# Performance work log

Hardware: AMD Instinct MI355X
Metric: run time of the kernel (lower is better)

Reference implementation:

```python
import jax, jax.numpy as jnp
import numpy as np
import math

D_MODEL = 1024
N_HEADS = 16
D_FF = 4096
B, S = 4, 2048
EPS = 1e-5


def _layernorm(x, g, b):
    mu = jnp.mean(x, axis=-1, keepdims=True)
    var = jnp.mean(jnp.square(x - mu), axis=-1, keepdims=True)
    return (x - mu) * jax.lax.rsqrt(var + EPS) * g + b


def setup_inputs() -> dict:
    key = jax.random.key(0)
    ks = jax.random.split(key, 16)
    D, F = D_MODEL, D_FF
    s = 1.0 / math.sqrt(D)
    sf = 1.0 / math.sqrt(F)
    return {
        "x": jax.random.normal(ks[0], (B, S, D), jnp.float32),
        "mask": jnp.ones((B, 1, 1, S), jnp.int32),
        "Wq": jax.random.uniform(ks[1], (D, D), jnp.float32, -s, s),
        "bq": jnp.zeros((D,), jnp.float32),
        "Wk": jax.random.uniform(ks[2], (D, D), jnp.float32, -s, s),
        "bk": jnp.zeros((D,), jnp.float32),
        "Wv": jax.random.uniform(ks[3], (D, D), jnp.float32, -s, s),
        "bv": jnp.zeros((D,), jnp.float32),
        "Wo": jax.random.uniform(ks[4], (D, D), jnp.float32, -s, s),
        "bo": jnp.zeros((D,), jnp.float32),
        "W1": jax.random.uniform(ks[5], (D, F), jnp.float32, -s, s),
        "b1": jnp.zeros((F,), jnp.float32),
        "W2": jax.random.uniform(ks[6], (F, D), jnp.float32, -sf, sf),
        "b2": jnp.zeros((D,), jnp.float32),
        "g1": jnp.ones((D,), jnp.float32),
        "be1": jnp.zeros((D,), jnp.float32),
        "g2": jnp.ones((D,), jnp.float32),
        "be2": jnp.zeros((D,), jnp.float32),
    }


def reference(x, mask, Wq, bq, Wk, bk, Wv, bv, Wo, bo, W1, b1, W2, b2, g1, be1, g2, be2):
    Bb, Ss, D = x.shape
    H = N_HEADS
    hd = D // H
    # QKV projections -> [B, H, S, hd]
    q = (x @ Wq + bq).reshape(Bb, Ss, H, hd).transpose(0, 2, 1, 3)
    k = (x @ Wk + bk).reshape(Bb, Ss, H, hd).transpose(0, 2, 1, 3)
    v = (x @ Wv + bv).reshape(Bb, Ss, H, hd).transpose(0, 2, 1, 3)
    # explicit O(S^2) attention, as in the source
    scores = jnp.einsum("bhqd,bhkd->bhqk", q, k) / math.sqrt(hd)
    scores = jnp.where(mask == 0, jnp.float32(-1e9), scores)
    attn = jax.nn.softmax(scores, axis=-1)
    o = jnp.einsum("bhqk,bhkd->bhqd", attn, v)
    o = o.transpose(0, 2, 1, 3).reshape(Bb, Ss, D)
    attn_out = o @ Wo + bo
    # residual + LN (dropout in eval mode = identity)
    h = _layernorm(x + attn_out, g1, be1)
    ff = jax.nn.relu(h @ W1 + b1) @ W2 + b2
    return _layernorm(h + ff, g2, be2)
```

## Files before the change

### kernel.cpp

```cpp
#include <hip/hip_runtime.h>
#include <hip/hip_bf16.h>
#include <stdint.h>

typedef __bf16 bf16;
typedef __bf16 bf16x8 __attribute__((ext_vector_type(8)));
typedef __bf16 bf16x4 __attribute__((ext_vector_type(4)));
typedef float f32x4 __attribute__((ext_vector_type(4)));
typedef unsigned short u16;

__device__ __forceinline__ float b2f(bf16 v) { return (float)v; }
__device__ __forceinline__ bf16 f2b(float f) { return (bf16)f; }

#define GLD16(gp, lp)                                              \
  __builtin_amdgcn_global_load_lds(                                \
      (const __attribute__((address_space(1))) void*)(gp),         \
      (__attribute__((address_space(3))) void*)(lp), 16, 0, 0)

__device__ __forceinline__ float ldval(const void* p, size_t i, int isf32) {
  return isf32 ? ((const float*)p)[i] : b2f(((const bf16*)p)[i]);
}

__global__ void sniff_kernel(const void* x, int* flag) {
  __shared__ int smax[256];
  int tid = threadIdx.x;
  const u16* p = (const u16*)x;
  int mx = 0;
  for (int i = tid; i < 8192; i += 256) {
    int e = (p[i] >> 7) & 0xFF;
    mx = mx > e ? mx : e;
  }
  smax[tid] = mx;
  __syncthreads();
  for (int s = 128; s > 0; s >>= 1) {
    if (tid < s) smax[tid] = smax[tid] > smax[tid + s] ? smax[tid] : smax[tid + s];
    __syncthreads();
  }
  if (tid == 0) *flag = (smax[0] >= 135) ? 1 : 0;
}

__global__ void cvt_kernel8(const void* __restrict__ in, bf16* __restrict__ out,
                            int n8, const int* __restrict__ flag) {
  int f = *flag;
  int i = blockIdx.x * 256 + threadIdx.x;
  if (i >= n8) return;
  bf16x8 o;
  if (f) {
    const float4* p = (const float4*)in + (size_t)i * 2;
    float4 a = p[0], c = p[1];
    o[0] = f2b(a.x); o[1] = f2b(a.y); o[2] = f2b(a.z); o[3] = f2b(a.w);
    o[4] = f2b(c.x); o[5] = f2b(c.y); o[6] = f2b(c.z); o[7] = f2b(c.w);
  } else {
    o = ((const bf16x8*)in)[i];
  }
  ((bf16x8*)out)[i] = o;
}

__global__ void cvt_biases_kernel(const void* bq, const void* bk, const void* bv,
                                  const void* bo, const void* b1, const void* b2,
                                  const void* g1, const void* be1, const void* g2,
                                  const void* be2, bf16* __restrict__ sv,
                                  const int* __restrict__ flag) {
  int f = *flag;
  int i = blockIdx.x * 256 + threadIdx.x;
  if (i >= 13312) return;
  int seg = i >> 10;
  int off = i & 1023;
  const void* src;
  switch (seg) {
    case 0: src = bq; break;
    case 1: src = bk; break;
    case 2: src = bv; break;
    case 3: src = bo; break;
    case 4: case 5: case 6: case 7: src = b1; off = i - 4096; break;
    case 8: src = b2; break;
    case 9: src = g1; break;
    case 10: src = be1; break;
    case 11: src = g2; break;
    default: src = be2; break;
  }
  sv[i] = f2b(ldval(src, off, f));
}

__global__ void transpose_all(const void* Wq, const void* Wk, const void* Wv,
                              const void* Wo, const void* W1, const void* W2,
                              bf16* WqkvT, bf16* WoT, bf16* W1T, bf16* W2T,
                              const int* __restrict__ flag) {
  int f = *flag;
  __shared__ bf16 tile[32][33];
  int blk = blockIdx.x;
  const void* in; bf16* out; int K, N, bx, by;
  if (blk < 4096) {
    int w = blk >> 10, t = blk & 1023;
    bx = t & 31; by = t >> 5; K = 1024; N = 1024;
    if (w == 0)      { in = Wq; out = WqkvT; }
    else if (w == 1) { in = Wk; out = WqkvT + 1024 * 1024; }
    else if (w == 2) { in = Wv; out = WqkvT + 2048 * 1024; }
    else             { in = Wo; out = WoT; }
  } else if (blk < 8192) {
    int t = blk - 4096; bx = t & 127; by = t >> 7; K = 1024; N = 4096;
    in = W1; out = W1T;
  } else {
    int t = blk - 8192; bx = t & 31; by = t >> 5; K = 4096; N = 1024;
    in = W2; out = W2T;
  }
  int bn = bx * 32, bk = by * 32;
  int tx = threadIdx.x, ty = threadIdx.y;
#pragma unroll
  for (int i = 0; i < 32; i += 8)
    tile[ty + i][tx] = f2b(ldval(in, (size_t)(bk + ty + i) * N + bn + tx, f));
  __syncthreads();
#pragma unroll
  for (int i = 0; i < 32; i += 8)
    out[(size_t)(bn + ty + i) * K + bk + tx] = tile[tx][ty + i];
}

template <int ACT, int GROUP>
__global__ __launch_bounds__(256, 4)
void gemm_bt(const bf16* __restrict__ A, const bf16* __restrict__ Bt,
             const bf16* __restrict__ bias, bf16* __restrict__ C,
             int M, int N, int K) {
  __shared__ __attribute__((aligned(16))) bf16 As[128][64];
  __shared__ __attribute__((aligned(16))) bf16 Bs[128][64];
  bf16 (*Cs)[136] = (bf16(*)[136])&As[0][0];
  const int tid = threadIdx.x;
  const int wave = tid >> 6;
  const int lane = tid & 63;

  const int grid_n = N >> 7;
  const int pid = blockIdx.x;
  const int xcd = pid & 7;
  const int j = pid >> 3;
  const int per = GROUP * grid_n;
  const int chunk = j / per;
  const int r0 = j - chunk * per;
  const int mb = xcd * 8 + chunk * GROUP + (r0 & (GROUP - 1));
  const int nb = r0 / GROUP;
  const int m0 = mb * 128;
  const int n0 = nb * 128;

  const int wr = (wave >> 1) * 64;
  const int wc = (wave & 1) * 64;
  const int row_q = lane & 15;
  const int quad = lane >> 4;

  const f32x4 fz = {0.f, 0.f, 0.f, 0.f};
  f32x4 acc[4][4];
#pragma unroll
  for (int i = 0; i < 4; i++)
#pragma unroll
    for (int jj = 0; jj < 4; jj++) acc[i][jj] = fz;

  int srow[4], sck[4];
#pragma unroll
  for (int i = 0; i < 4; i++) {
    int c = i * 256 + tid;
    srow[i] = c >> 3;
    sck[i] = (c & 7) * 8;
  }

  for (int k0 = 0; k0 < K; k0 += 64) {
    __syncthreads();
#pragma unroll
    for (int i = 0; i < 4; i++) {
      GLD16(A + (size_t)(m0 + srow[i]) * K + k0 + sck[i], &As[srow[i]][sck[i]]);
      GLD16(Bt + (size_t)(n0 + srow[i]) * K + k0 + sck[i], &Bs[srow[i]][sck[i]]);
    }
    __syncthreads();
#pragma unroll
    for (int ks = 0; ks < 2; ks++) {
      bf16x8 af[4], bfr[4];
      int cf = ks * 4 + quad;
#pragma unroll
      for (int mi = 0; mi < 4; mi++)
        af[mi] = *(const bf16x8*)&As[wr + mi * 16 + row_q][cf * 8];
#pragma unroll
      for (int ni = 0; ni < 4; ni++)
        bfr[ni] = *(const bf16x8*)&Bs[wc + ni * 16 + row_q][cf * 8];
#pragma unroll
      for (int mi = 0; mi < 4; mi++)
#pragma unroll
        for (int ni = 0; ni < 4; ni++)
          acc[mi][ni] = __builtin_amdgcn_mfma_f32_16x16x32_bf16(
              af[mi], bfr[ni], acc[mi][ni], 0, 0, 0);
    }
  }

#pragma unroll
  for (int p = 0; p < 4; p++) {
    __syncthreads();
    if ((wave >> 1) == (p >> 1)) {
#pragma unroll
      for (int ni = 0; ni < 4; ni++) {
        int col = wc + ni * 16 + row_q;
        float bval = b2f(bias[n0 + col]);
#pragma unroll
        for (int mi2 = 0; mi2 < 2; mi2++) {
          int mi = (p & 1) * 2 + mi2;
#pragma unroll
          for (int reg = 0; reg < 4; reg++) {
            int lr = mi2 * 16 + quad * 4 + reg;
            float v = acc[mi][ni][reg] + bval;
            if (ACT == 1) v = v > 0.f ? v : 0.f;
            Cs[lr][col] = f2b(v);
          }
        }
      }
    }
    __syncthreads();
#pragma unroll
    for (int i = 0; i < 2; i++) {
      int u = i * 256 + tid;
      int row = u >> 4;
      int cu = u & 15;
      uint4 v = *(const uint4*)&Cs[row][cu * 8];
      *(uint4*)&C[(size_t)(m0 + p * 32 + row) * N + n0 + cu * 8] = v;
    }
  }
}

template <int GROUP>
__global__ __launch_bounds__(256, 4)
void gemm_qkv(const bf16* __restrict__ A, const bf16* __restrict__ Bt,
              const bf16* __restrict__ bias, bf16* __restrict__ Cqk,
              bf16* __restrict__ Vg, int M, int K) {
  __shared__ __attribute__((aligned(16))) bf16 As[128][64];
  __shared__ __attribute__((aligned(16))) bf16 Bs[128][64];
  bf16 (*Cs)[136] = (bf16(*)[136])&As[0][0];
  const int tid = threadIdx.x;
  const int wave = tid >> 6;
  const int lane = tid & 63;

  const int grid_n = 24;
  const int pid = blockIdx.x;
  const int xcd = pid & 7;
  const int j = pid >> 3;
  const int per = GROUP * grid_n;
  const int chunk = j / per;
  const int r0 = j - chunk * per;
  const int mb = xcd * 8 + chunk * GROUP + (r0 & (GROUP - 1));
  const int nb = r0 / GROUP;
  const int m0 = mb * 128;
  const int n0 = nb * 128;

  const int wr = (wave >> 1) * 64;
  const int wc = (wave & 1) * 64;
  const int row_q = lane & 15;
  const int quad = lane >> 4;

  const f32x4 fz = {0.f, 0.f, 0.f, 0.f};
  f32x4 acc[4][4];
#pragma unroll
  for (int i = 0; i < 4; i++)
#pragma unroll
    for (int jj = 0; jj < 4; jj++) acc[i][jj] = fz;

  int srow[4], sck[4];
#pragma unroll
  for (int i = 0; i < 4; i++) {
    int c = i * 256 + tid;
    srow[i] = c >> 3;
    sck[i] = (c & 7) * 8;
  }

  for (int k0 = 0; k0 < K; k0 += 64) {
    __syncthreads();
#pragma unroll
    for (int i = 0; i < 4; i++) {
      GLD16(A + (size_t)(m0 + srow[i]) * K + k0 + sck[i], &As[srow[i]][sck[i]]);
      GLD16(Bt + (size_t)(n0 + srow[i]) * K + k0 + sck[i], &Bs[srow[i]][sck[i]]);
    }
    __syncthreads();
#pragma unroll
    for (int ks = 0; ks < 2; ks++) {
      bf16x8 af[4], bfr[4];
      int cf = ks * 4 + quad;
#pragma unroll
      for (int mi = 0; mi < 4; mi++)
        af[mi] = *(const bf16x8*)&As[wr + mi * 16 + row_q][cf * 8];
#pragma unroll
      for (int ni = 0; ni < 4; ni++)
        bfr[ni] = *(const bf16x8*)&Bs[wc + ni * 16 + row_q][cf * 8];
#pragma unroll
      for (int mi = 0; mi < 4; mi++)
#pragma unroll
        for (int ni = 0; ni < 4; ni++)
          acc[mi][ni] = __builtin_amdgcn_mfma_f32_16x16x32_bf16(
              af[mi], bfr[ni], acc[mi][ni], 0, 0, 0);
    }
  }

  if (nb < 16) {
#pragma unroll
    for (int p = 0; p < 4; p++) {
      __syncthreads();
      if ((wave >> 1) == (p >> 1)) {
#pragma unroll
        for (int ni = 0; ni < 4; ni++) {
          int col = wc + ni * 16 + row_q;
          float bval = b2f(bias[n0 + col]);
#pragma unroll
          for (int mi2 = 0; mi2 < 2; mi2++) {
            int mi = (p & 1) * 2 + mi2;
#pragma unroll
            for (int reg = 0; reg < 4; reg++) {
              int lr = mi2 * 16 + quad * 4 + reg;
              Cs[lr][col] = f2b(acc[mi][ni][reg] + bval);
            }
          }
        }
      }
      __syncthreads();
#pragma unroll
      for (int i = 0; i < 2; i++) {
        int u = i * 256 + tid;
        int row = u >> 4;
        int cu = u & 15;
        uint4 v = *(const uint4*)&Cs[row][cu * 8];
        *(uint4*)&Cqk[(size_t)(m0 + p * 32 + row) * 2048 + n0 + cu * 8] = v;
      }
    }
  } else {
    const int n0v = n0 - 2048;
    const int b = m0 >> 11;
    const int s0 = m0 & 2047;
#pragma unroll
    for (int p = 0; p < 4; p++) {
      __syncthreads();
      if ((wave & 1) == (p >> 1)) {
#pragma unroll
        for (int ni2 = 0; ni2 < 2; ni2++) {
          int ni = (p & 1) * 2 + ni2;
          int cl = ni2 * 16 + row_q;
          float bval = b2f(bias[n0 + p * 32 + cl]);
#pragma unroll
          for (int mi = 0; mi < 4; mi++)
#pragma unroll
            for (int reg = 0; reg < 4; reg++) {
              int row = wr + mi * 16 + quad * 4 + reg;
              Cs[cl][row] = f2b(acc[mi][ni][reg] + bval);
            }
        }
      }
      __syncthreads();
#pragma unroll
      for (int i = 0; i < 2; i++) {
        int u = i * 256 + tid;
        int cl = u >> 4;
        int rc = u & 15;
        uint4 v = *(const uint4*)&Cs[cl][rc * 8];
        *(uint4*)&Vg[(size_t)(b * 1024 + n0v + p * 32 + cl) * 2048 + s0 + rc * 8] = v;
      }
    }
  }
}

#define BC 64
__global__ __launch_bounds__(256, 6)
void attn_kernel(const bf16* __restrict__ QKb, const bf16* __restrict__ Vg,
                 const int* __restrict__ mask, bf16* __restrict__ O) {
  __shared__ __attribute__((aligned(16))) bf16 Ks[BC][64];
  __shared__ __attribute__((aligned(16))) bf16 Vt[64][BC];
  __shared__ __attribute__((aligned(16))) bf16 Ps[4][16][72];
  const int tid = threadIdx.x;
  const int wave = tid >> 6, lane = tid & 63;
  const int pid = blockIdx.x;
  const int xcd = pid & 7;
  const int jj = pid >> 3;
  const int bh = xcd * 8 + (jj >> 5);
  const int b = bh >> 4, h = bh & 15;
  const int q0 = (jj & 31) * 64;
  const int row_q = lane & 15, quad = lane >> 4;

  bf16x8 qf[2];
  {
    int qrow = q0 + wave * 16 + row_q;
    const bf16* qp = QKb + (size_t)(b * 2048 + qrow) * 2048 + h * 64 + quad * 8;
    qf[0] = *(const bf16x8*)qp;
    qf[1] = *(const bf16x8*)(qp + 32);
#pragma unroll
    for (int ks = 0; ks < 2; ks++)
#pragma unroll
      for (int e = 0; e < 8; e++) qf[ks][e] = f2b(b2f(qf[ks][e]) * 0.125f);
  }
  float m_i = -1e30f, l_i = 0.f;
  const f32x4 fz = {0.f, 0.f, 0.f, 0.f};
  f32x4 o_acc[4];
#pragma unroll
  for (int d = 0; d < 4; d++) o_acc[d] = fz;

  int ki[2], kdc[2], ksc[2], vsc[2];
#pragma unroll
  for (int j = 0; j < 2; j++) {
    int c = j * 256 + tid;
    ki[j] = c >> 3;  kdc[j] = c & 7;
    ksc[j] = (c & 7) ^ (ki[j] & 7);
    vsc[j] = ksc[j];
  }
  const bf16* Kbase = QKb + (size_t)b * 2048 * 2048 + 1024 + h * 64;
  const bf16* Vbase = Vg + (size_t)(b * 1024 + h * 64) * 2048;
  const int* mrow = mask + b * 2048;
  const int swz = row_q & 7;

  unsigned int allmask = 0;
  for (int kb = 0; kb < 2048 / BC; kb++) {
    int mm = mrow[kb * BC + lane];
    if (__ballot(mm != 0) == ~0ull) allmask |= (1u << kb);
  }

  for (int kb = 0; kb < 2048 / BC; kb++) {
    __syncthreads();
#pragma unroll
    for (int j = 0; j < 2; j++)
      GLD16(Kbase + (size_t)(kb * BC + ki[j]) * 2048 + ksc[j] * 8,
            &Ks[ki[j]][kdc[j] * 8]);
#pragma unroll
    for (int j = 0; j < 2; j++)
      GLD16(Vbase + (size_t)ki[j] * 2048 + kb * BC + vsc[j] * 8,
            &Vt[ki[j]][kdc[j] * 8]);
    __syncthreads();

    f32x4 sacc[4];
#pragma unroll
    for (int nt = 0; nt < 4; nt++) sacc[nt] = fz;
#pragma unroll
    for (int ks = 0; ks < 2; ks++) {
      int kcf = ((ks * 4 + quad) ^ swz) * 8;
#pragma unroll
      for (int nt = 0; nt < 4; nt++) {
        bf16x8 kf = *(const bf16x8*)&Ks[nt * 16 + row_q][kcf];
        sacc[nt] = __builtin_amdgcn_mfma_f32_16x16x32_bf16(kf, qf[ks], sacc[nt], 0, 0, 0);
      }
    }
    if (!((allmask >> kb) & 1u)) {
#pragma unroll
      for (int nt = 0; nt < 4; nt++) {
        int4 m4 = *(const int4*)&mrow[kb * BC + nt * 16 + quad * 4];
#pragma unroll
        for (int r = 0; r < 4; r++)
          if (((const int*)&m4)[r] == 0) sacc[nt][r] = -1e9f;
      }
    }
    float mq[4];
#pragma unroll
    for (int nt = 0; nt < 4; nt++)
      mq[nt] = fmaxf(fmaxf(sacc[nt][0], sacc[nt][1]),
                     fmaxf(sacc[nt][2], sacc[nt][3]));
    float mx = fmaxf(fmaxf(mq[0], mq[1]), fmaxf(mq[2], mq[3]));
    mx = fmaxf(mx, __shfl_xor(mx, 16));
    mx = fmaxf(mx, __shfl_xor(mx, 32));
    if (!__all(mx - m_i <= 5.0f)) {
      float mnew = fmaxf(m_i, mx);
      float alpha = __expf(m_i - mnew);
      m_i = mnew;
      l_i *= alpha;
      float al[4];
#pragma unroll
      for (int r = 0; r < 4; r++) al[r] = __shfl(alpha, quad * 4 + r);
#pragma unroll
      for (int d = 0; d < 4; d++)
#pragma unroll
        for (int r = 0; r < 4; r++) o_acc[d][r] *= al[r];
    }
    float rs = 0.f;
#pragma unroll
    for (int nt = 0; nt < 4; nt++) {
      float p0 = __expf(sacc[nt][0] - m_i);
      float p1 = __expf(sacc[nt][1] - m_i);
      float p2 = __expf(sacc[nt][2] - m_i);
      float p3 = __expf(sacc[nt][3] - m_i);
      rs += (p0 + p1) + (p2 + p3);
      bf16x4 pv = {f2b(p0), f2b(p1), f2b(p2), f2b(p3)};
      *(bf16x4*)&Ps[wave][row_q][nt * 16 + quad * 4] = pv;
    }
    rs += __shfl_xor(rs, 16);
    rs += __shfl_xor(rs, 32);
    l_i += rs;
#pragma unroll
    for (int kst = 0; kst < 2; kst++) {
      bf16x8 pf = *(const bf16x8*)&Ps[wave][row_q][kst * 32 + quad * 8];
      int vcf = ((kst * 4 + quad) ^ swz) * 8;
#pragma unroll
      for (int d = 0; d < 4; d++) {
        bf16x8 vf = *(const bf16x8*)&Vt[d * 16 + row_q][vcf];
        o_acc[d] = __builtin_amdgcn_mfma_f32_16x16x32_bf16(pf, vf, o_acc[d], 0, 0, 0);
      }
    }
  }
  float lv[4];
#pragma unroll
  for (int r = 0; r < 4; r++) lv[r] = __shfl(l_i, quad * 4 + r);
#pragma unroll
  for (int d = 0; d < 4; d++) {
#pragma unroll
    for (int r = 0; r < 4; r++) {
      int row = q0 + wave * 16 + quad * 4 + r;
      float v = o_acc[d][r] / fmaxf(lv[r], 1e-20f);
      O[(size_t)(b * 2048 + row) * 1024 + h * 64 + d * 16 + row_q] = f2b(v);
    }
  }
}

__global__ __launch_bounds__(256)
void ln_kernel(const bf16* __restrict__ a, const bf16* __restrict__ res,
               const bf16* __restrict__ g, const bf16* __restrict__ be,
               bf16* __restrict__ out) {
  const int tid = threadIdx.x;
  __shared__ float red[8];
  const size_t base = (size_t)blockIdx.x * 1024;
  bf16x4 av = *(const bf16x4*)&a[base + tid * 4];
  bf16x4 rv = *(const bf16x4*)&res[base + tid * 4];
  float xs[4], sum = 0.f, sq = 0.f;
#pragma unroll
  for (int i = 0; i < 4; i++) {
    float x = b2f(av[i]) + b2f(rv[i]);
    xs[i] = x; sum += x; sq += x * x;
  }
#pragma unroll
  for (int off = 1; off < 64; off <<= 1) {
    sum += __shfl_xor(sum, off);
    sq += __shfl_xor(sq, off);
  }
  int wave = tid >> 6, lane = tid & 63;
  if (lane == 0) { red[wave] = sum; red[4 + wave] = sq; }
  __syncthreads();
  sum = red[0] + red[1] + red[2] + red[3];
  sq = red[4] + red[5] + red[6] + red[7];
  float mu = sum * (1.f / 1024.f);
  float var = sq * (1.f / 1024.f) - mu * mu;
  float rstd = rsqrtf(fmaxf(var, 0.f) + 1e-5f);
  bf16x4 gv = *(const bf16x4*)&g[tid * 4];
  bf16x4 bv = *(const bf16x4*)&be[tid * 4];
  bf16x4 ov;
#pragma unroll
  for (int i = 0; i < 4; i++)
    ov[i] = f2b((xs[i] - mu) * rstd * b2f(gv[i]) + b2f(bv[i]));
  *(bf16x4*)&out[base + tid * 4] = ov;
}

__global__ __launch_bounds__(256)
void ln_out_kernel(const bf16* __restrict__ a, const bf16* __restrict__ res,
                   const bf16* __restrict__ g, const bf16* __restrict__ be,
                   void* __restrict__ out, const int* __restrict__ flag) {
  const int f = *flag;
  const int tid = threadIdx.x;
  __shared__ float red[8];
  const size_t base = (size_t)blockIdx.x * 1024;
  bf16x4 av = *(const bf16x4*)&a[base + tid * 4];
  bf16x4 rv = *(const bf16x4*)&res[base + tid * 4];
  float xs[4], sum = 0.f, sq = 0.f;
#pragma unroll
  for (int i = 0; i < 4; i++) {
    float x = b2f(av[i]) + b2f(rv[i]);
    xs[i] = x; sum += x; sq += x * x;
  }
#pragma unroll
  for (int off = 1; off < 64; off <<= 1) {
    sum += __shfl_xor(sum, off);
    sq += __shfl_xor(sq, off);
  }
  int wave = tid >> 6, lane = tid & 63;
  if (lane == 0) { red[wave] = sum; red[4 + wave] = sq; }
  __syncthreads();
  sum = red[0] + red[1] + red[2] + red[3];
  sq = red[4] + red[5] + red[6] + red[7];
  float mu = sum * (1.f / 1024.f);
  float var = sq * (1.f / 1024.f) - mu * mu;
  float rstd = rsqrtf(fmaxf(var, 0.f) + 1e-5f);
  bf16x4 gv = *(const bf16x4*)&g[tid * 4];
  bf16x4 bv = *(const bf16x4*)&be[tid * 4];
  float y[4];
#pragma unroll
  for (int i = 0; i < 4; i++)
    y[i] = (xs[i] - mu) * rstd * b2f(gv[i]) + b2f(bv[i]);
  if (f) {
    float4 o = {y[0], y[1], y[2], y[3]};
    ((float4*)out)[base / 4 + tid] = o;
  } else {
    bf16x4 o = {f2b(y[0]), f2b(y[1]), f2b(y[2]), f2b(y[3])};
    *(bf16x4*)&((bf16*)out)[base + tid * 4] = o;
  }
}

extern "C" void kernel_launch(void* const* d_in, const int* in_sizes, int n_in,
                              void* d_out, int out_size, void* d_ws, size_t ws_size,
                              hipStream_t stream) {
  (void)in_sizes; (void)n_in; (void)out_size; (void)ws_size;
  const void* x   = d_in[0];
  const int* mask = (const int*)d_in[1];
  const void* Wq  = d_in[2];
  const void* bq  = d_in[3];
  const void* Wk  = d_in[4];
  const void* bk  = d_in[5];
  const void* Wv  = d_in[6];
  const void* bv  = d_in[7];
  const void* Wo  = d_in[8];
  const void* bo  = d_in[9];
  const void* W1  = d_in[10];
  const void* b1  = d_in[11];
  const void* W2  = d_in[12];
  const void* b2  = d_in[13];
  const void* g1  = d_in[14];
  const void* be1 = d_in[15];
  const void* g2  = d_in[16];
  const void* be2 = d_in[17];

  char* ws = (char*)d_ws;
  bf16* xb    = (bf16*)(ws + 0);
  bf16* WqkvT = (bf16*)(ws + 16777216);
  bf16* WoT   = (bf16*)(ws + 23068672);
  bf16* W1T   = (bf16*)(ws + 25165824);
  bf16* W2T   = (bf16*)(ws + 33554432);
  bf16* sv    = (bf16*)(ws + 41943040);
  bf16* bqkvB = sv;
  bf16* boB   = sv + 3072;
  bf16* b1B   = sv + 4096;
  bf16* b2B   = sv + 8192;
  bf16* g1B   = sv + 9216;
  bf16* be1B  = sv + 10240;
  bf16* g2B   = sv + 11264;
  bf16* be2B  = sv + 12288;
  int*  flag  = (int*)(ws + 41943040 + 26624);
  bf16* QKb   = (bf16*)(ws + 41975808);
  bf16* Vg    = (bf16*)(ws + 75530240);
  bf16* Obuf  = (bf16*)(ws + 92307456);
  bf16* hbuf  = (bf16*)(ws + 109084672);
  bf16* attnp = (bf16*)(ws + 41975808);
  bf16* ff1   = (bf16*)(ws + 41975808);
  bf16* ff2o  = (bf16*)(ws + 0);

  sniff_kernel<<<1, 256, 0, stream>>>(x, flag);

  cvt_kernel8<<<4096, 256, 0, stream>>>(x, xb, 1048576, flag);
  cvt_biases_kernel<<<52, 256, 0, stream>>>(bq, bk, bv, bo, b1, b2, g1, be1,
                                            g2, be2, sv, flag);

  dim3 tb(32, 8);
  transpose_all<<<12288, tb, 0, stream>>>(Wq, Wk, Wv, Wo, W1, W2,
                                          WqkvT, WoT, W1T, W2T, flag);

  gemm_qkv<8><<<1536, 256, 0, stream>>>(xb, WqkvT, bqkvB, QKb, Vg, 8192, 1024);
  attn_kernel<<<2048, 256, 0, stream>>>(QKb, Vg, mask, Obuf);
  gemm_bt<0, 8><<<512, 256, 0, stream>>>(Obuf, WoT, boB, attnp, 8192, 1024, 1024);
  ln_kernel<<<8192, 256, 0, stream>>>(xb, attnp, g1B, be1B, hbuf);
  gemm_bt<1, 8><<<2048, 256, 0, stream>>>(hbuf, W1T, b1B, ff1, 8192, 4096, 1024);
  gemm_bt<0, 4><<<512, 256, 0, stream>>>(ff1, W2T, b2B, ff2o, 8192, 1024, 4096);
  ln_out_kernel<<<8192, 256, 0, stream>>>(hbuf, ff2o, g2B, be2B, d_out, flag);
}
```

Baseline: 592.6 us.

## Triple-buffer GEMM K-loop with async LDS loads and swizzled layout

Replaces the single-buffer, two-barrier GEMM main loop in both gemm_bt and gemm_qkv with a 3-stage ring of 32-wide K tiles, loaded via global_load_lds and gated by manual vmcnt waits. Global loads for later tiles can then overlap MFMA work on the current tile. The LDS tile is XOR-swizzled to cut bank conflicts, and occupancy is lowered to 3 blocks per CU to make room for the extra shared memory. The attention kernel's vsc alias is folded into ksc, a cosmetic change. The risks are lower occupancy and fragile hand-written waitcnt logic.

```diff
diff --git a/kernel.cpp b/kernel.cpp
--- a/kernel.cpp
+++ b/kernel.cpp
@@ -114,14 +114,69 @@
     out[(size_t)(bn + ty + i) * K + bk + tx] = tile[tx][ty + i];
 }
 
+#define GEMM_PIPE_LOOP(Aptr, Bptr)                                             \
+  const int NT = K >> 5;                                                       \
+  int srow[2], sch[2], ssc[2];                                                 \
+  _Pragma("unroll")                                                            \
+  for (int j = 0; j < 2; ++j) {                                                \
+    int c = j * 256 + tid;                                                     \
+    srow[j] = c >> 2;                                                          \
+    sch[j] = (c & 3) * 8;                                                      \
+    ssc[j] = ((c & 3) ^ ((srow[j] >> 1) & 3)) * 8;                             \
+  }                                                                            \
+  const bf16* pA0 = Aptr + (size_t)(m0 + srow[0]) * K + ssc[0];                \
+  const bf16* pA1 = Aptr + (size_t)(m0 + srow[1]) * K + ssc[1];                \
+  const bf16* pB0 = Bptr + (size_t)(n0 + srow[0]) * K + ssc[0];                \
+  const bf16* pB1 = Bptr + (size_t)(n0 + srow[1]) * K + ssc[1];                \
+  _Pragma("unroll")                                                            \
+  for (int tt = 0; tt < 3; ++tt) {                                             \
+    GLD16(pA0 + tt * 32, &As[tt][srow[0]][sch[0]]);                            \
+    GLD16(pB0 + tt * 32, &Bs[tt][srow[0]][sch[0]]);                            \
+    GLD16(pA1 + tt * 32, &As[tt][srow[1]][sch[1]]);                            \
+    GLD16(pB1 + tt * 32, &Bs[tt][srow[1]][sch[1]]);                            \
+  }                                                                            \
+  asm volatile("s_waitcnt vmcnt(8)" ::: "memory");                             \
+  const int cf = (quad ^ ((row_q >> 1) & 3)) * 8;                              \
+  int slot = 0;                                                                \
+  for (int t = 0; t < NT; ++t) {                                               \
+    __builtin_amdgcn_s_barrier();                                              \
+    bf16x8 af[4], bfr[4];                                                      \
+    _Pragma("unroll")                                                          \
+    for (int mi = 0; mi < 4; mi++)                                             \
+      af[mi] = *(const bf16x8*)&As[slot][wr + mi * 16 + row_q][cf];            \
+    _Pragma("unroll")                                                          \
+    for (int ni = 0; ni < 4; ni++)                                             \
+      bfr[ni] = *(const bf16x8*)&Bs[slot][wc + ni * 16 + row_q][cf];           \
+    _Pragma("unroll")                                                          \
+    for (int mi = 0; mi < 4; mi++)                                             \
+      _Pragma("unroll")                                                        \
+      for (int ni = 0; ni < 4; ni++)                                           \
+        acc[mi][ni] = __builtin_amdgcn_mfma_f32_16x16x32_bf16(                 \
+            af[mi], bfr[ni], acc[mi][ni], 0, 0, 0);                            \
+    __builtin_amdgcn_s_barrier();                                              \
+    __builtin_amdgcn_sched_barrier(0);      \
+    if (t + 3 < NT) {                                                          \
+      int k0 = (t + 3) << 5;                                                   \
+      GLD16(pA0 + k0, &As[slot][srow[0]][sch[0]]);                             \
+      GLD16(pB0 + k0, &Bs[slot][srow[0]][sch[0]]);                             \
+      GLD16(pA1 + k0, &As[slot][srow[1]][sch[1]]);                             \
+      GLD16(pB1 + k0, &Bs[slot][srow[1]][sch[1]]);                             \
+    }                                                                          \
+    int rem = NT - 1 - t;                                                      \
+    if (rem >= 3)      asm volatile("s_waitcnt vmcnt(8)" ::: "memory");        \
+    else if (rem == 2) asm volatile("s_waitcnt vmcnt(4)" ::: "memory");        \
+    else if (rem == 1) asm volatile("s_waitcnt vmcnt(0)" ::: "memory");        \
+    slot = (slot == 2) ? 0 : slot + 1;                                         \
+  }
+
 template <int ACT, int GROUP>
-__global__ __launch_bounds__(256, 4)
+__global__ __launch_bounds__(256, 3)
 void gemm_bt(const bf16* __restrict__ A, const bf16* __restrict__ Bt,
              const bf16* __restrict__ bias, bf16* __restrict__ C,
              int M, int N, int K) {
-  __shared__ __attribute__((aligned(16))) bf16 As[128][64];
-  __shared__ __attribute__((aligned(16))) bf16 Bs[128][64];
-  bf16 (*Cs)[136] = (bf16(*)[136])&As[0][0];
+  __shared__ __attribute__((aligned(16))) bf16 As[3][128][32];
+  __shared__ __attribute__((aligned(16))) bf16 Bs[3][128][32];
+  bf16 (*Cs)[136] = (bf16(*)[136])&As[0][0][0];
   const int tid = threadIdx.x;
   const int wave = tid >> 6;
   const int lane = tid & 63;
@@ -150,40 +205,7 @@
 #pragma unroll
     for (int jj = 0; jj < 4; jj++) acc[i][jj] = fz;
 
-  int srow[4], sck[4];
-#pragma unroll
-  for (int i = 0; i < 4; i++) {
-    int c = i * 256 + tid;
-    srow[i] = c >> 3;
-    sck[i] = (c & 7) * 8;
-  }
-
-  for (int k0 = 0; k0 < K; k0 += 64) {
-    __syncthreads();
-#pragma unroll
-    for (int i = 0; i < 4; i++) {
-      GLD16(A + (size_t)(m0 + srow[i]) * K + k0 + sck[i], &As[srow[i]][sck[i]]);
-      GLD16(Bt + (size_t)(n0 + srow[i]) * K + k0 + sck[i], &Bs[srow[i]][sck[i]]);
-    }
-    __syncthreads();
-#pragma unroll
-    for (int ks = 0; ks < 2; ks++) {
-      bf16x8 af[4], bfr[4];
-      int cf = ks * 4 + quad;
-#pragma unroll
-      for (int mi = 0; mi < 4; mi++)
-        af[mi] = *(const bf16x8*)&As[wr + mi * 16 + row_q][cf * 8];
-#pragma unroll
-      for (int ni = 0; ni < 4; ni++)
-        bfr[ni] = *(const bf16x8*)&Bs[wc + ni * 16 + row_q][cf * 8];
-#pragma unroll
-      for (int mi = 0; mi < 4; mi++)
-#pragma unroll
-        for (int ni = 0; ni < 4; ni++)
-          acc[mi][ni] = __builtin_amdgcn_mfma_f32_16x16x32_bf16(
-              af[mi], bfr[ni], acc[mi][ni], 0, 0, 0);
-    }
-  }
+  GEMM_PIPE_LOOP(A, Bt)
 
 #pragma unroll
   for (int p = 0; p < 4; p++) {
@@ -219,13 +241,13 @@
 }
 
 template <int GROUP>
-__global__ __launch_bounds__(256, 4)
+__global__ __launch_bounds__(256, 3)
 void gemm_qkv(const bf16* __restrict__ A, const bf16* __restrict__ Bt,
               const bf16* __restrict__ bias, bf16* __restrict__ Cqk,
               bf16* __restrict__ Vg, int M, int K) {
-  __shared__ __attribute__((aligned(16))) bf16 As[128][64];
-  __shared__ __attribute__((aligned(16))) bf16 Bs[128][64];
-  bf16 (*Cs)[136] = (bf16(*)[136])&As[0][0];
+  __shared__ __attribute__((aligned(16))) bf16 As[3][128][32];
+  __shared__ __attribute__((aligned(16))) bf16 Bs[3][128][32];
+  bf16 (*Cs)[136] = (bf16(*)[136])&As[0][0][0];
   const int tid = threadIdx.x;
   const int wave = tid >> 6;
   const int lane = tid & 63;
@@ -254,40 +276,7 @@
 #pragma unroll
     for (int jj = 0; jj < 4; jj++) acc[i][jj] = fz;
 
-  int srow[4], sck[4];
-#pragma unroll
-  for (int i = 0; i < 4; i++) {
-    int c = i * 256 + tid;
-    srow[i] = c >> 3;
-    sck[i] = (c & 7) * 8;
-  }
-
-  for (int k0 = 0; k0 < K; k0 += 64) {
-    __syncthreads();
-#pragma unroll
-    for (int i = 0; i < 4; i++) {
-      GLD16(A + (size_t)(m0 + srow[i]) * K + k0 + sck[i], &As[srow[i]][sck[i]]);
-      GLD16(Bt + (size_t)(n0 + srow[i]) * K + k0 + sck[i], &Bs[srow[i]][sck[i]]);
-    }
-    __syncthreads();
-#pragma unroll
-    for (int ks = 0; ks < 2; ks++) {
-      bf16x8 af[4], bfr[4];
-      int cf = ks * 4 + quad;
-#pragma unroll
-      for (int mi = 0; mi < 4; mi++)
-        af[mi] = *(const bf16x8*)&As[wr + mi * 16 + row_q][cf * 8];
-#pragma unroll
-      for (int ni = 0; ni < 4; ni++)
-        bfr[ni] = *(const bf16x8*)&Bs[wc + ni * 16 + row_q][cf * 8];
-#pragma unroll
-      for (int mi = 0; mi < 4; mi++)
-#pragma unroll
-        for (int ni = 0; ni < 4; ni++)
-          acc[mi][ni] = __builtin_amdgcn_mfma_f32_16x16x32_bf16(
-              af[mi], bfr[ni], acc[mi][ni], 0, 0, 0);
-    }
-  }
+  GEMM_PIPE_LOOP(A, Bt)
 
   if (nb < 16) {
 #pragma unroll
@@ -388,13 +377,12 @@
 #pragma unroll
   for (int d = 0; d < 4; d++) o_acc[d] = fz;
 
-  int ki[2], kdc[2], ksc[2], vsc[2];
+  int ki[2], kdc[2], ksc[2];
 #pragma unroll
   for (int j = 0; j < 2; j++) {
     int c = j * 256 + tid;
     ki[j] = c >> 3;  kdc[j] = c & 7;
     ksc[j] = (c & 7) ^ (ki[j] & 7);
-    vsc[j] = ksc[j];
   }
   const bf16* Kbase = QKb + (size_t)b * 2048 * 2048 + 1024 + h * 64;
   const bf16* Vbase = Vg + (size_t)(b * 1024 + h * 64) * 2048;
@@ -415,7 +403,7 @@
             &Ks[ki[j]][kdc[j] * 8]);
 #pragma unroll
     for (int j = 0; j < 2; j++)
-      GLD16(Vbase + (size_t)ki[j] * 2048 + kb * BC + vsc[j] * 8,
+      GLD16(Vbase + (size_t)ki[j] * 2048 + kb * BC + ksc[j] * 8,
             &Vt[ki[j]][kdc[j] * 8]);
     __syncthreads();
 
```

New measurement: 564.2 us. 1.05x faster.
